# Kernel tuning notes

Hardware: AMD Instinct MI355X
Metric: run time of the kernel (lower is better)

Reference implementation:

```python
import jax, jax.numpy as jnp
import numpy as np

B, T_MEL, T_TXT = 16, 2048, 1024
D_MODEL, D_ENC_M, D_ENC_T = 512, 512, 512
LN_EPS = 1e-5


def setup_inputs() -> dict:
    key = jax.random.key(0)
    ks = jax.random.split(key, 9)
    mel_encoding = jax.random.normal(ks[0], (B, T_MEL, D_ENC_M), dtype=jnp.float32)
    text_encoding = jax.random.normal(ks[1], (B, T_TXT, D_ENC_T), dtype=jnp.float32)
    mel_mask = jax.random.randint(ks[2], (B, T_MEL), 0, 2).astype(bool)
    mel_mask = mel_mask.at[:, 0].set(False)  # guarantee >=1 unmasked key per row
    src_mask = jax.random.randint(ks[3], (B, T_TXT), 0, 2).astype(bool)
    # Projection weights stored [in, out] (torch Linear does x @ W.T)
    sc = 1.0 / np.sqrt(D_ENC_M)
    Wq = jax.random.uniform(ks[4], (D_ENC_T, D_MODEL), jnp.float32, -sc, sc)
    Wk = jax.random.uniform(ks[5], (D_ENC_M, D_MODEL), jnp.float32, -sc, sc)
    Wv = jax.random.uniform(ks[6], (D_ENC_M, D_MODEL), jnp.float32, -sc, sc)
    ln_gamma = jnp.ones((D_MODEL,), jnp.float32)
    ln_beta = jnp.zeros((D_MODEL,), jnp.float32)
    return {"mel_encoding": mel_encoding, "text_encoding": text_encoding,
            "mel_mask": mel_mask, "src_mask": src_mask,
            "Wq": Wq, "Wk": Wk, "Wv": Wv,
            "ln_gamma": ln_gamma, "ln_beta": ln_beta}


def reference(mel_encoding, text_encoding, mel_mask, src_mask, Wq, Wk, Wv, ln_gamma, ln_beta):
    temperature = jnp.sqrt(jnp.float32(D_ENC_M))
    q = jnp.einsum('btd,dm->btm', text_encoding, Wq)   # [B, T_txt, d_model]
    k = jnp.einsum('bsd,dm->bsm', mel_encoding, Wk)    # [B, T_mel, d_model]
    v = jnp.einsum('bsd,dm->bsm', mel_encoding, Wv)
    # attn_mask = outer product of src_mask and mel_mask (True -> masked)
    attn_mask = src_mask[:, :, None] & mel_mask[:, None, :]  # [B, T_txt, T_mel]
    scores = jnp.einsum('btm,bsm->bts', q, k) / temperature
    scores = jnp.where(attn_mask, -jnp.inf, scores)
    attn = jax.nn.softmax(scores, axis=2)
    output = jnp.einsum('bts,bsm->btm', attn, v)
    # dropout is identity at inference; LayerNorm over last dim
    mean = jnp.mean(output, axis=-1, keepdims=True)
    var = jnp.var(output, axis=-1, keepdims=True)
    output = (output - mean) * jax.lax.rsqrt(var + LN_EPS) * ln_gamma + ln_beta
    return output, attn
```

## Files before the change

### kernel.cpp

```cpp
#include <hip/hip_runtime.h>

#define DEV __device__ __forceinline__

typedef __attribute__((ext_vector_type(8))) short short8v;
typedef __attribute__((ext_vector_type(4))) float f32x4;

DEV unsigned short f2bf(float f) {
  unsigned int x = __float_as_uint(f);
  x = x + 0x7FFFu + ((x >> 16) & 1u);
  return (unsigned short)(x >> 16);
}
DEV float bf2f(unsigned short u) {
  return __uint_as_float(((unsigned)u) << 16);
}

DEV int swz_byte(int row, int kElem) {
  int chunk = ((kElem >> 3) ^ (row & 7));
  return row * 128 + (chunk << 4) + ((kElem & 7) << 1);
}

template <int ROUNDS>
DEV void stage(const unsigned short* __restrict__ g, int ld,
               unsigned short* tile, int tid) {
  const int wave = tid >> 6, l = tid & 63;
#pragma unroll
  for (int p = 0; p < ROUNDS; ++p) {
    const int r = (p << 5) + (wave << 3) + (l >> 3);
    const int c = ((l & 7) ^ (r & 7)) << 3;
    const unsigned short* src = g + (long)r * ld + c;
#if __has_builtin(__builtin_amdgcn_global_load_lds)
    unsigned short* dst = tile + (p << 11) + (wave << 9);
    __builtin_amdgcn_global_load_lds(
        (const __attribute__((address_space(1))) void*)src,
        (__attribute__((address_space(3))) void*)dst, 16, 0, 0);
#else
    short8v v = *reinterpret_cast<const short8v*>(src);
    *reinterpret_cast<short8v*>(reinterpret_cast<char*>(tile) +
                                (p << 12) + (wave << 10) + (l << 4)) = v;
#endif
  }
}

template <int BM>
DEV void stage_f32(const float* __restrict__ g, int ld,
                   unsigned short* tile, int tid) {
  const int rl = tid >> 4;
  const int c4 = (tid & 15) << 2;
#pragma unroll
  for (int p = 0; p < BM / 16; ++p) {
    const int row = (p << 4) + rl;
    const float4 f = *reinterpret_cast<const float4*>(g + (long)row * ld + c4);
    ushort4 pack;
    pack.x = f2bf(f.x); pack.y = f2bf(f.y); pack.z = f2bf(f.z); pack.w = f2bf(f.w);
    *reinterpret_cast<ushort4*>(reinterpret_cast<char*>(tile) +
                                swz_byte(row, c4)) = pack;
  }
}

template <int BM, int EPI, int GM, bool AF32>
__global__ __launch_bounds__(256) void gemm_bf16(
    const void* __restrict__ Av, const unsigned short* __restrict__ B,
    void* __restrict__ Cout, int M, int N, int K,
    long aBatch, long bBatch, long cBatch,
    const int* __restrict__ srcMask, const int* __restrict__ melMask,
    float scale, float* __restrict__ stats) {
  constexpr int NI = BM / 32;
  __shared__ unsigned short As[BM * 64];
  __shared__ unsigned short Bs[128 * 64];
  const int tid = threadIdx.x;
  const int lane = tid & 63;
  const int wave = tid >> 6;
  int z, bmi, bni;
  if constexpr (GM == 1) {
    const int id = blockIdx.x;
    z = (id & 7) | ((id >> 10) << 3);
    const int ib = (id >> 3) & 127;
    bni = ib & 15;
    bmi = ib >> 4;
  } else if constexpr (GM == 2) {
    bmi = blockIdx.x; bni = blockIdx.y; z = blockIdx.z;
  } else {
    bni = blockIdx.x; bmi = blockIdx.y; z = blockIdx.z;
  }
  const int bm = bmi * BM;
  const int bn = bni * 128;
  const unsigned short* Bb = B + (long)z * bBatch;
  const long cOff = (long)z * cBatch;
  const int wr = (wave >> 1) * (BM / 2);
  const int wc = (wave & 1) * 64;
  const int l15 = lane & 15;
  const int lHi = lane >> 4;

  f32x4 acc[NI][4] = {};

  for (int kt = 0; kt < K; kt += 64) {
    if constexpr (AF32) {
      stage_f32<BM>((const float*)Av + (long)z * aBatch + (long)bm * K + kt, K, As, tid);
    } else {
      stage<BM / 32>((const unsigned short*)Av + (long)z * aBatch + (long)bm * K + kt,
                     K, As, tid);
    }
    stage<4>(Bb + (long)bn * K + kt, K, Bs, tid);
    __syncthreads();
#pragma unroll
    for (int ks = 0; ks < 2; ++ks) {
      const int k0 = (ks << 5) + (lHi << 3);
      short8v af[NI], bfr[4];
#pragma unroll
      for (int i = 0; i < NI; ++i)
        af[i] = *reinterpret_cast<const short8v*>(
            reinterpret_cast<const char*>(As) + swz_byte(wr + i * 16 + l15, k0));
#pragma unroll
      for (int j = 0; j < 4; ++j)
        bfr[j] = *reinterpret_cast<const short8v*>(
            reinterpret_cast<const char*>(Bs) + swz_byte(wc + j * 16 + l15, k0));
#pragma unroll
      for (int i = 0; i < NI; ++i)
#pragma unroll
        for (int j = 0; j < 4; ++j)
          acc[i][j] = __builtin_amdgcn_mfma_f32_16x16x32_bf16(af[i], bfr[j], acc[i][j], 0, 0, 0);
    }
    __syncthreads();
  }

  if constexpr (EPI == 2) {
    __shared__ float redM[128][2];
    __shared__ float redS[128][2];
    const int wcIdx = wave & 1;
#pragma unroll
    for (int i = 0; i < NI; ++i) {
#pragma unroll
      for (int rr = 0; rr < 4; ++rr) {
        const int rloc = wr + i * 16 + lHi * 4 + rr;
        const int rb = bm + rloc;
        const bool sm = srcMask[z * 1024 + rb] != 0;
        float vals[4];
        float m_l = -3.0e38f;
#pragma unroll
        for (int j = 0; j < 4; ++j) {
          const int c = bn + wc + j * 16 + l15;
          const bool mm = melMask[z * 2048 + c] != 0;
          const float vf = (sm && mm) ? -1e30f : acc[i][j][rr] * scale;
          vals[j] = vf;
          reinterpret_cast<unsigned short*>(Cout)[cOff + (long)rb * N + c] = f2bf(vf);
          m_l = fmaxf(m_l, vf);
        }
#pragma unroll
        for (int o = 1; o < 16; o <<= 1) m_l = fmaxf(m_l, __shfl_xor(m_l, o, 64));
        float s_l = 0.f;
#pragma unroll
        for (int j = 0; j < 4; ++j) s_l += __expf(vals[j] - m_l);
#pragma unroll
        for (int o = 1; o < 16; o <<= 1) s_l += __shfl_xor(s_l, o, 64);
        if (l15 == 0) { redM[rloc][wcIdx] = m_l; redS[rloc][wcIdx] = s_l; }
      }
    }
    __syncthreads();
    if (tid < 128) {
      const float m0 = redM[tid][0], m1 = redM[tid][1];
      const float Mx = fmaxf(m0, m1);
      const float S = redS[tid][0] * __expf(m0 - Mx) + redS[tid][1] * __expf(m1 - Mx);
      const long sidx = ((long)(z * 1024 + bm + tid)) * 32 + (long)bni * 2;
      stats[sidx] = Mx;
      stats[sidx + 1] = S;
    }
  } else {
#pragma unroll
    for (int i = 0; i < NI; ++i) {
#pragma unroll
      for (int j = 0; j < 4; ++j) {
        const int rb = bm + wr + i * 16 + lHi * 4;
        const int c = bn + wc + j * 16 + l15;
#pragma unroll
        for (int r = 0; r < 4; ++r) {
          const long idx = cOff + (long)(rb + r) * N + c;
          reinterpret_cast<unsigned short*>(Cout)[idx] = f2bf(acc[i][j][r]);
        }
      }
    }
  }
}

__global__ __launch_bounds__(256) void attn_write(
    const unsigned short* __restrict__ sbf, const float* __restrict__ stats,
    float* __restrict__ attn) {
  const long row = blockIdx.x;
  const float* st = stats + row * 32;
  float Mx = -3.0e38f;
#pragma unroll
  for (int t = 0; t < 16; ++t) Mx = fmaxf(Mx, st[t * 2]);
  float S = 0.f;
#pragma unroll
  for (int t = 0; t < 16; ++t) S += st[t * 2 + 1] * __expf(st[t * 2] - Mx);
  const float inv = 1.0f / S;
  const long base = row * 2048 + threadIdx.x * 8;
  const short8v s = *reinterpret_cast<const short8v*>(sbf + base);
  float4 w0, w1;
  w0.x = __expf(bf2f((unsigned short)s[0]) - Mx) * inv;
  w0.y = __expf(bf2f((unsigned short)s[1]) - Mx) * inv;
  w0.z = __expf(bf2f((unsigned short)s[2]) - Mx) * inv;
  w0.w = __expf(bf2f((unsigned short)s[3]) - Mx) * inv;
  w1.x = __expf(bf2f((unsigned short)s[4]) - Mx) * inv;
  w1.y = __expf(bf2f((unsigned short)s[5]) - Mx) * inv;
  w1.z = __expf(bf2f((unsigned short)s[6]) - Mx) * inv;
  w1.w = __expf(bf2f((unsigned short)s[7]) - Mx) * inv;
  *reinterpret_cast<float4*>(attn + base) = w0;
  *reinterpret_cast<float4*>(attn + base + 4) = w1;
}

__global__ __launch_bounds__(256) void pv(
    const unsigned short* __restrict__ sbf, const unsigned short* __restrict__ vT,
    float* __restrict__ out, const float* __restrict__ stats) {
  __shared__ unsigned short As[64 * 64];
  __shared__ unsigned short Bs[128 * 64];
  __shared__ float rowM[64], rowInv[64];
  const int id = blockIdx.x;
  const int z = (id & 7) | ((id >> 9) << 3);
  const int ib = (id >> 3) & 63;
  const int mt = ib & 15, nt = ib >> 4;
  const int bm = mt * 64, bn = nt * 128;
  const int tid = threadIdx.x, lane = tid & 63, wave = tid >> 6;

  if (tid < 64) {
    const float* st = stats + ((long)(z * 1024 + bm + tid)) * 32;
    float Mx = -3.0e38f;
#pragma unroll
    for (int t = 0; t < 16; ++t) Mx = fmaxf(Mx, st[t * 2]);
    float S = 0.f;
#pragma unroll
    for (int t = 0; t < 16; ++t) S += st[t * 2 + 1] * __expf(st[t * 2] - Mx);
    rowM[tid] = Mx;
    rowInv[tid] = 1.0f / S;
  }
  __syncthreads();

  const int ar = tid >> 2;
  const int ac = (tid & 3) << 4;
  const float mR = rowM[ar];
  const float invR = rowInv[ar];
  const long aOff = ((long)z * 1024 + bm + ar) * 2048 + ac;
  const unsigned short* vTb = vT + ((long)z * 512 + bn) * 2048;
  const int wr = (wave >> 1) * 32, wc = (wave & 1) * 64;
  const int l15 = lane & 15, lHi = lane >> 4;

  f32x4 acc[2][4] = {};
  short8v s0 = *reinterpret_cast<const short8v*>(sbf + aOff);
  short8v s1 = *reinterpret_cast<const short8v*>(sbf + aOff + 8);

  for (int kt = 0; kt < 2048; kt += 64) {
    stage<4>(vTb + kt, 2048, Bs, tid);
    short8v pk0, pk1;
#pragma unroll
    for (int u = 0; u < 8; ++u) {
      pk0[u] = (short)f2bf(__expf(bf2f((unsigned short)s0[u]) - mR) * invR);
      pk1[u] = (short)f2bf(__expf(bf2f((unsigned short)s1[u]) - mR) * invR);
    }
    *reinterpret_cast<short8v*>(reinterpret_cast<char*>(As) + swz_byte(ar, ac)) = pk0;
    *reinterpret_cast<short8v*>(reinterpret_cast<char*>(As) + swz_byte(ar, ac + 8)) = pk1;
    if (kt < 2048 - 64) {
      s0 = *reinterpret_cast<const short8v*>(sbf + aOff + kt + 64);
      s1 = *reinterpret_cast<const short8v*>(sbf + aOff + kt + 72);
    }
    __syncthreads();

#pragma unroll
    for (int ks = 0; ks < 2; ++ks) {
      const int k0 = (ks << 5) + (lHi << 3);
      short8v af[2], bfr[4];
#pragma unroll
      for (int i = 0; i < 2; ++i)
        af[i] = *reinterpret_cast<const short8v*>(
            reinterpret_cast<const char*>(As) + swz_byte(wr + i * 16 + l15, k0));
#pragma unroll
      for (int j = 0; j < 4; ++j)
        bfr[j] = *reinterpret_cast<const short8v*>(
            reinterpret_cast<const char*>(Bs) + swz_byte(wc + j * 16 + l15, k0));
#pragma unroll
      for (int i = 0; i < 2; ++i)
#pragma unroll
        for (int j = 0; j < 4; ++j)
          acc[i][j] = __builtin_amdgcn_mfma_f32_16x16x32_bf16(af[i], bfr[j], acc[i][j], 0, 0, 0);
    }
    __syncthreads();
  }

#pragma unroll
  for (int i = 0; i < 2; ++i)
#pragma unroll
    for (int j = 0; j < 4; ++j) {
      const int row = bm + wr + i * 16 + lHi * 4;
      const int col = bn + wc + j * 16 + l15;
#pragma unroll
      for (int rr = 0; rr < 4; ++rr)
        out[((long)z * 1024 + row + rr) * 512 + col] = acc[i][j][rr];
    }
}

__global__ __launch_bounds__(256) void f32_to_bf16(
    const float* __restrict__ in, unsigned short* __restrict__ out, long n) {
  long i = ((long)blockIdx.x * blockDim.x + threadIdx.x) * 8;
  const long stride = (long)gridDim.x * blockDim.x * 8;
  for (; i < n; i += stride) {
    const float4 a = *reinterpret_cast<const float4*>(in + i);
    const float4 b = *reinterpret_cast<const float4*>(in + i + 4);
    short8v o;
    o[0] = (short)f2bf(a.x); o[1] = (short)f2bf(a.y);
    o[2] = (short)f2bf(a.z); o[3] = (short)f2bf(a.w);
    o[4] = (short)f2bf(b.x); o[5] = (short)f2bf(b.y);
    o[6] = (short)f2bf(b.z); o[7] = (short)f2bf(b.w);
    *reinterpret_cast<short8v*>(out + i) = o;
  }
}

__global__ __launch_bounds__(256) void conv_w2(
    const float* __restrict__ Wq, const float* __restrict__ Wk,
    unsigned short* __restrict__ wqbf, unsigned short* __restrict__ wkbf) {
  const float* in = blockIdx.y ? Wk : Wq;
  unsigned short* out = blockIdx.y ? wkbf : wqbf;
  const long i = ((long)blockIdx.x * 256 + threadIdx.x) * 8;
  const float4 a = *reinterpret_cast<const float4*>(in + i);
  const float4 b = *reinterpret_cast<const float4*>(in + i + 4);
  short8v o;
  o[0] = (short)f2bf(a.x); o[1] = (short)f2bf(a.y);
  o[2] = (short)f2bf(a.z); o[3] = (short)f2bf(a.w);
  o[4] = (short)f2bf(b.x); o[5] = (short)f2bf(b.y);
  o[6] = (short)f2bf(b.z); o[7] = (short)f2bf(b.w);
  *reinterpret_cast<short8v*>(out + i) = o;
}

__global__ __launch_bounds__(256) void transpose_wv(
    const float* __restrict__ Wv, unsigned short* __restrict__ WvT) {
  __shared__ float t[32][33];
  const int bx = blockIdx.x * 32;
  const int by = blockIdx.y * 32;
  const int tx = threadIdx.x, ty = threadIdx.y;
#pragma unroll
  for (int i = 0; i < 4; ++i)
    t[ty + i * 8][tx] = Wv[(long)(by + ty + i * 8) * 512 + bx + tx];
  __syncthreads();
#pragma unroll
  for (int i = 0; i < 4; ++i)
    WvT[(long)(bx + ty + i * 8) * 512 + by + tx] = f2bf(t[tx][ty + i * 8]);
}

__global__ __launch_bounds__(64) void layernorm_rows(
    float* __restrict__ out, const float* __restrict__ gamma, const float* __restrict__ beta) {
  const long row = blockIdx.x;
  float4* p = reinterpret_cast<float4*>(out + row * 512);
  const int lane = threadIdx.x;
  float4 a = p[lane];
  float4 b = p[lane + 64];
  float s = ((a.x + a.y) + (a.z + a.w)) + ((b.x + b.y) + (b.z + b.w));
  float s2 = ((a.x * a.x + a.y * a.y) + (a.z * a.z + a.w * a.w)) +
             ((b.x * b.x + b.y * b.y) + (b.z * b.z + b.w * b.w));
#pragma unroll
  for (int o = 32; o; o >>= 1) {
    s += __shfl_xor(s, o, 64);
    s2 += __shfl_xor(s2, o, 64);
  }
  const float mean = s * (1.0f / 512.0f);
  const float var = s2 * (1.0f / 512.0f) - mean * mean;
  const float rstd = rsqrtf(var + 1e-5f);
  const float4 g0 = reinterpret_cast<const float4*>(gamma)[lane];
  const float4 g1 = reinterpret_cast<const float4*>(gamma)[lane + 64];
  const float4 c0 = reinterpret_cast<const float4*>(beta)[lane];
  const float4 c1 = reinterpret_cast<const float4*>(beta)[lane + 64];
  a.x = (a.x - mean) * rstd * g0.x + c0.x;
  a.y = (a.y - mean) * rstd * g0.y + c0.y;
  a.z = (a.z - mean) * rstd * g0.z + c0.z;
  a.w = (a.w - mean) * rstd * g0.w + c0.w;
  b.x = (b.x - mean) * rstd * g1.x + c1.x;
  b.y = (b.y - mean) * rstd * g1.y + c1.y;
  b.z = (b.z - mean) * rstd * g1.z + c1.z;
  b.w = (b.w - mean) * rstd * g1.w + c1.w;
  p[lane] = a;
  p[lane + 64] = b;
}

extern "C" void kernel_launch(void* const* d_in, const int* in_sizes, int n_in,
                              void* d_out, int out_size, void* d_ws, size_t ws_size,
                              hipStream_t stream) {
  const float* mel  = (const float*)d_in[0];
  const float* text = (const float*)d_in[1];
  const int* melMask = (const int*)d_in[2];
  const int* srcMask = (const int*)d_in[3];
  const float* Wq = (const float*)d_in[4];
  const float* Wk = (const float*)d_in[5];
  const float* Wv = (const float*)d_in[6];
  const float* gamma = (const float*)d_in[7];
  const float* beta  = (const float*)d_in[8];

  float* out = (float*)d_out;
  float* attn = (float*)d_out + (long)16 * 1024 * 512;

  unsigned short* ws = (unsigned short*)d_ws;
  unsigned short* wqbf = ws;
  unsigned short* wkbf = wqbf + 512 * 512;
  unsigned short* wvT  = wkbf + 512 * 512;
  unsigned short* Mt   = wvT + 512 * 512;
  unsigned short* melbf = Mt + 512 * 512;
  unsigned short* qbf  = melbf + (long)16 * 2048 * 512;
  unsigned short* vT   = qbf + (long)16 * 1024 * 512;
  unsigned short* sbf  = vT + (long)16 * 512 * 2048;
  float* stats = (float*)(sbf + (long)16 * 1024 * 2048);

  conv_w2<<<dim3(128, 2), 256, 0, stream>>>(Wq, Wk, wqbf, wkbf);
  transpose_wv<<<dim3(16, 16), dim3(32, 8), 0, stream>>>(Wv, wvT);
  f32_to_bf16<<<dim3(4096), 256, 0, stream>>>(mel, melbf, (long)16 * 2048 * 512);

  gemm_bf16<128, 0, 0, false><<<dim3(4, 4, 1), 256, 0, stream>>>(
      wkbf, wqbf, Mt, 512, 512, 512, 0, 0, 0, nullptr, nullptr, 1.0f, nullptr);
  gemm_bf16<128, 0, 2, true><<<dim3(128, 4, 1), 256, 0, stream>>>(
      text, Mt, qbf, 16384, 512, 512, 0, 0, 0, nullptr, nullptr, 1.0f, nullptr);
  gemm_bf16<128, 0, 0, false><<<dim3(16, 4, 16), 256, 0, stream>>>(
      wvT, melbf, vT, 512, 2048, 512, 0, (long)2048 * 512, (long)512 * 2048,
      nullptr, nullptr, 1.0f, nullptr);
  gemm_bf16<128, 2, 1, false><<<dim3(2048), 256, 0, stream>>>(
      qbf, melbf, sbf, 1024, 2048, 512,
      (long)1024 * 512, (long)2048 * 512, (long)1024 * 2048,
      srcMask, melMask, 0.044194173824159216f, stats);
  attn_write<<<dim3(16 * 1024), 256, 0, stream>>>(sbf, stats, attn);
  pv<<<dim3(1024), 256, 0, stream>>>(sbf, vT, out, stats);
  layernorm_rows<<<dim3(16 * 1024), 64, 0, stream>>>(out, gamma, beta);
}
```

Before: 273.2 us.

## Fuse softmax attn output write into PV kernel and merge weight prep kernels

```diff
diff --git a/kernel.cpp b/kernel.cpp
--- a/kernel.cpp
+++ b/kernel.cpp
@@ -181,38 +181,12 @@
   }
 }
 
-__global__ __launch_bounds__(256) void attn_write(
-    const unsigned short* __restrict__ sbf, const float* __restrict__ stats,
-    float* __restrict__ attn) {
-  const long row = blockIdx.x;
-  const float* st = stats + row * 32;
-  float Mx = -3.0e38f;
-#pragma unroll
-  for (int t = 0; t < 16; ++t) Mx = fmaxf(Mx, st[t * 2]);
-  float S = 0.f;
-#pragma unroll
-  for (int t = 0; t < 16; ++t) S += st[t * 2 + 1] * __expf(st[t * 2] - Mx);
-  const float inv = 1.0f / S;
-  const long base = row * 2048 + threadIdx.x * 8;
-  const short8v s = *reinterpret_cast<const short8v*>(sbf + base);
-  float4 w0, w1;
-  w0.x = __expf(bf2f((unsigned short)s[0]) - Mx) * inv;
-  w0.y = __expf(bf2f((unsigned short)s[1]) - Mx) * inv;
-  w0.z = __expf(bf2f((unsigned short)s[2]) - Mx) * inv;
-  w0.w = __expf(bf2f((unsigned short)s[3]) - Mx) * inv;
-  w1.x = __expf(bf2f((unsigned short)s[4]) - Mx) * inv;
-  w1.y = __expf(bf2f((unsigned short)s[5]) - Mx) * inv;
-  w1.z = __expf(bf2f((unsigned short)s[6]) - Mx) * inv;
-  w1.w = __expf(bf2f((unsigned short)s[7]) - Mx) * inv;
-  *reinterpret_cast<float4*>(attn + base) = w0;
-  *reinterpret_cast<float4*>(attn + base + 4) = w1;
-}
-
-__global__ __launch_bounds__(256) void pv(
+__global__ __launch_bounds__(256) void pv_smx(
     const unsigned short* __restrict__ sbf, const unsigned short* __restrict__ vT,
-    float* __restrict__ out, const float* __restrict__ stats) {
-  __shared__ unsigned short As[64 * 64];
-  __shared__ unsigned short Bs[128 * 64];
+    float* __restrict__ attn, float* __restrict__ out,
+    const float* __restrict__ stats) {
+  __shared__ unsigned short As[2][64 * 64];
+  __shared__ unsigned short Bs[2][128 * 64];
   __shared__ float rowM[64], rowInv[64];
   const int id = blockIdx.x;
   const int z = (id & 7) | ((id >> 9) << 3);
@@ -244,42 +218,62 @@
   const int l15 = lane & 15, lHi = lane >> 4;
 
   f32x4 acc[2][4] = {};
-  short8v s0 = *reinterpret_cast<const short8v*>(sbf + aOff);
-  short8v s1 = *reinterpret_cast<const short8v*>(sbf + aOff + 8);
-
-  for (int kt = 0; kt < 2048; kt += 64) {
-    stage<4>(vTb + kt, 2048, Bs, tid);
-    short8v pk0, pk1;
-#pragma unroll
-    for (int u = 0; u < 8; ++u) {
-      pk0[u] = (short)f2bf(__expf(bf2f((unsigned short)s0[u]) - mR) * invR);
-      pk1[u] = (short)f2bf(__expf(bf2f((unsigned short)s1[u]) - mR) * invR);
-    }
-    *reinterpret_cast<short8v*>(reinterpret_cast<char*>(As) + swz_byte(ar, ac)) = pk0;
-    *reinterpret_cast<short8v*>(reinterpret_cast<char*>(As) + swz_byte(ar, ac + 8)) = pk1;
-    if (kt < 2048 - 64) {
-      s0 = *reinterpret_cast<const short8v*>(sbf + aOff + kt + 64);
-      s1 = *reinterpret_cast<const short8v*>(sbf + aOff + kt + 72);
-    }
-    __syncthreads();
-
-#pragma unroll
-    for (int ks = 0; ks < 2; ++ks) {
-      const int k0 = (ks << 5) + (lHi << 3);
-      short8v af[2], bfr[4];
-#pragma unroll
-      for (int i = 0; i < 2; ++i)
-        af[i] = *reinterpret_cast<const short8v*>(
-            reinterpret_cast<const char*>(As) + swz_byte(wr + i * 16 + l15, k0));
-#pragma unroll
-      for (int j = 0; j < 4; ++j)
-        bfr[j] = *reinterpret_cast<const short8v*>(
-            reinterpret_cast<const char*>(Bs) + swz_byte(wc + j * 16 + l15, k0));
-#pragma unroll
-      for (int i = 0; i < 2; ++i)
+
+  for (int it = 0; it < 16; ++it) {
+    const int kt = it << 7;
+    stage<4>(vTb + kt, 2048, Bs[0], tid);
+    stage<4>(vTb + kt + 64, 2048, Bs[1], tid);
+#pragma unroll
+    for (int h = 0; h < 2; ++h) {
+      const int kh = kt + (h << 6);
+      const short8v s0 = *reinterpret_cast<const short8v*>(sbf + aOff + kh);
+      const short8v s1 = *reinterpret_cast<const short8v*>(sbf + aOff + kh + 8);
+      float e[16];
+#pragma unroll
+      for (int u = 0; u < 8; ++u) {
+        e[u] = __expf(bf2f((unsigned short)s0[u]) - mR) * invR;
+        e[u + 8] = __expf(bf2f((unsigned short)s1[u]) - mR) * invR;
+      }
+      if ((kh >> 9) == nt) {
+        float* ap = attn + aOff + kh;
+#pragma unroll
+        for (int g = 0; g < 4; ++g) {
+          float4 w;
+          w.x = e[g * 4]; w.y = e[g * 4 + 1]; w.z = e[g * 4 + 2]; w.w = e[g * 4 + 3];
+          *reinterpret_cast<float4*>(ap + g * 4) = w;
+        }
+      }
+      short8v pk0, pk1;
+#pragma unroll
+      for (int u = 0; u < 8; ++u) {
+        pk0[u] = (short)f2bf(e[u]);
+        pk1[u] = (short)f2bf(e[u + 8]);
+      }
+      *reinterpret_cast<short8v*>(reinterpret_cast<char*>(As[h]) + swz_byte(ar, ac)) = pk0;
+      *reinterpret_cast<short8v*>(reinterpret_cast<char*>(As[h]) + swz_byte(ar, ac + 8)) = pk1;
+    }
+    __syncthreads();
+
+#pragma unroll
+    for (int h = 0; h < 2; ++h) {
+#pragma unroll
+      for (int ks = 0; ks < 2; ++ks) {
+        const int k0 = (ks << 5) + (lHi << 3);
+        short8v af[2], bfr[4];
+#pragma unroll
+        for (int i = 0; i < 2; ++i)
+          af[i] = *reinterpret_cast<const short8v*>(
+              reinterpret_cast<const char*>(As[h]) + swz_byte(wr + i * 16 + l15, k0));
 #pragma unroll
         for (int j = 0; j < 4; ++j)
-          acc[i][j] = __builtin_amdgcn_mfma_f32_16x16x32_bf16(af[i], bfr[j], acc[i][j], 0, 0, 0);
+          bfr[j] = *reinterpret_cast<const short8v*>(
+              reinterpret_cast<const char*>(Bs[h]) + swz_byte(wc + j * 16 + l15, k0));
+#pragma unroll
+        for (int i = 0; i < 2; ++i)
+#pragma unroll
+          for (int j = 0; j < 4; ++j)
+            acc[i][j] = __builtin_amdgcn_mfma_f32_16x16x32_bf16(af[i], bfr[j], acc[i][j], 0, 0, 0);
+      }
     }
     __syncthreads();
   }
@@ -312,35 +306,32 @@
   }
 }
 
-__global__ __launch_bounds__(256) void conv_w2(
+__global__ __launch_bounds__(256) void prep_w(
     const float* __restrict__ Wq, const float* __restrict__ Wk,
-    unsigned short* __restrict__ wqbf, unsigned short* __restrict__ wkbf) {
-  const float* in = blockIdx.y ? Wk : Wq;
-  unsigned short* out = blockIdx.y ? wkbf : wqbf;
-  const long i = ((long)blockIdx.x * 256 + threadIdx.x) * 8;
-  const float4 a = *reinterpret_cast<const float4*>(in + i);
-  const float4 b = *reinterpret_cast<const float4*>(in + i + 4);
-  short8v o;
-  o[0] = (short)f2bf(a.x); o[1] = (short)f2bf(a.y);
-  o[2] = (short)f2bf(a.z); o[3] = (short)f2bf(a.w);
-  o[4] = (short)f2bf(b.x); o[5] = (short)f2bf(b.y);
-  o[6] = (short)f2bf(b.z); o[7] = (short)f2bf(b.w);
-  *reinterpret_cast<short8v*>(out + i) = o;
-}
-
-__global__ __launch_bounds__(256) void transpose_wv(
-    const float* __restrict__ Wv, unsigned short* __restrict__ WvT) {
-  __shared__ float t[32][33];
-  const int bx = blockIdx.x * 32;
-  const int by = blockIdx.y * 32;
+    const float* __restrict__ Wv, unsigned short* __restrict__ wqbf,
+    unsigned short* __restrict__ wkbf, unsigned short* __restrict__ WvT) {
+  const int zz = blockIdx.z;
   const int tx = threadIdx.x, ty = threadIdx.y;
-#pragma unroll
-  for (int i = 0; i < 4; ++i)
-    t[ty + i * 8][tx] = Wv[(long)(by + ty + i * 8) * 512 + bx + tx];
-  __syncthreads();
-#pragma unroll
-  for (int i = 0; i < 4; ++i)
-    WvT[(long)(bx + ty + i * 8) * 512 + by + tx] = f2bf(t[tx][ty + i * 8]);
+  if (zz == 0) {
+    __shared__ float t[32][33];
+    const int bx = blockIdx.x * 32;
+    const int by = blockIdx.y * 32;
+#pragma unroll
+    for (int i = 0; i < 4; ++i)
+      t[ty + i * 8][tx] = Wv[(long)(by + ty + i * 8) * 512 + bx + tx];
+    __syncthreads();
+#pragma unroll
+    for (int i = 0; i < 4; ++i)
+      WvT[(long)(bx + ty + i * 8) * 512 + by + tx] = f2bf(t[tx][ty + i * 8]);
+  } else {
+    const float* in = (zz == 1) ? Wq : Wk;
+    unsigned short* out = (zz == 1) ? wqbf : wkbf;
+    const long base = ((long)(blockIdx.y * 16 + blockIdx.x) * 256 + ty * 32 + tx) * 4;
+    const float4 f = *reinterpret_cast<const float4*>(in + base);
+    ushort4 o;
+    o.x = f2bf(f.x); o.y = f2bf(f.y); o.z = f2bf(f.z); o.w = f2bf(f.w);
+    *reinterpret_cast<ushort4*>(out + base) = o;
+  }
 }
 
 __global__ __launch_bounds__(64) void layernorm_rows(
@@ -404,8 +395,7 @@
   unsigned short* sbf  = vT + (long)16 * 512 * 2048;
   float* stats = (float*)(sbf + (long)16 * 1024 * 2048);
 
-  conv_w2<<<dim3(128, 2), 256, 0, stream>>>(Wq, Wk, wqbf, wkbf);
-  transpose_wv<<<dim3(16, 16), dim3(32, 8), 0, stream>>>(Wv, wvT);
+  prep_w<<<dim3(16, 16, 3), dim3(32, 8), 0, stream>>>(Wq, Wk, Wv, wqbf, wkbf, wvT);
   f32_to_bf16<<<dim3(4096), 256, 0, stream>>>(mel, melbf, (long)16 * 2048 * 512);
 
   gemm_bf16<128, 0, 0, false><<<dim3(4, 4, 1), 256, 0, stream>>>(
@@ -419,7 +409,6 @@
       qbf, melbf, sbf, 1024, 2048, 512,
       (long)1024 * 512, (long)2048 * 512, (long)1024 * 2048,
       srcMask, melMask, 0.044194173824159216f, stats);
-  attn_write<<<dim3(16 * 1024), 256, 0, stream>>>(sbf, stats, attn);
-  pv<<<dim3(1024), 256, 0, stream>>>(sbf, vT, out, stats);
+  pv_smx<<<dim3(1024), 256, 0, stream>>>(sbf, vT, attn, out, stats);
   layernorm_rows<<<dim3(16 * 1024), 64, 0, stream>>>(out, gamma, beta);
 }
```

After: 261.0 us. 1.05x faster.
